# Optimization experiments

Hardware: AMD Instinct MI355X
Metric: run time of the kernel (lower is better)

## Reference

```python
import jax, jax.numpy as jnp
import numpy as np

N_NODES = 100000
N_EDGES = 1600000
IN_CH = 64
HID = 64
OUT_CH = 16


def setup_inputs() -> dict:
    key = jax.random.key(0)
    ks = jax.random.split(key, 8)
    x = jax.random.normal(ks[0], (N_NODES, IN_CH), dtype=jnp.float32)
    edge_index = jax.random.randint(ks[1], (2, N_EDGES), 0, N_NODES, dtype=jnp.int64)
    s = 1.0 / np.sqrt(IN_CH)
    W1l = jax.random.normal(ks[2], (HID, IN_CH), dtype=jnp.float32) * s
    W1r = jax.random.normal(ks[3], (HID, IN_CH), dtype=jnp.float32) * s
    b1 = jnp.zeros((HID,), dtype=jnp.float32)
    W2l = jax.random.normal(ks[4], (HID, HID), dtype=jnp.float32) * s
    W2r = jax.random.normal(ks[5], (HID, HID), dtype=jnp.float32) * s
    b2 = jnp.zeros((HID,), dtype=jnp.float32)
    Wlin = jax.random.normal(ks[6], (OUT_CH, HID), dtype=jnp.float32) * s
    blin = jnp.zeros((OUT_CH,), dtype=jnp.float32)
    return {"x": x, "edge_index": edge_index, "W1l": W1l, "b1": b1, "W1r": W1r,
            "W2l": W2l, "b2": b2, "W2r": W2r, "Wlin": Wlin, "blin": blin}


def _sage_conv(x, src, dst, Wl, b, Wr):
    # PyG SAGEConv with mean aggregation:
    # out = lin_l(mean_{j in N(i)} x_j) + lin_r(x_i); bias lives in lin_l.
    msgs = x[src]                                              # [E, F] gather
    summed = jax.ops.segment_sum(msgs, dst, num_segments=N_NODES)  # [N, F]
    cnt = jax.ops.segment_sum(jnp.ones((src.shape[0],), x.dtype), dst,
                              num_segments=N_NODES)            # [N]
    agg = summed / jnp.maximum(cnt, 1.0)[:, None]              # mean, deg-0 safe
    return agg @ Wl.T + b + x @ Wr.T


def reference(x, edge_index, W1l, b1, W1r, W2l, b2, W2r, Wlin, blin):
    src, dst = edge_index[0], edge_index[1]
    h = jax.nn.relu(_sage_conv(x, src, dst, W1l, b1, W1r))
    h = jax.nn.relu(_sage_conv(h, src, dst, W2l, b2, W2r))
    return h @ Wlin.T + blin
```

## Files before the change

kernel.cpp:

```cpp
#include <hip/hip_runtime.h>

#define NN 100000
#define NE 1600000

#define BSHIFT 9
#define BWIDTH (1 << BSHIFT)
#define NBUCK ((NN + BWIDTH - 1) >> BSHIFT)
#define SLOTS 12288
#define CHUNK 4096
#define B1_BLOCKS ((NE + CHUNK - 1) / CHUNK)
#define GEMM_BLOCKS ((NN + 63) / 64)

typedef float    v2f __attribute__((ext_vector_type(2)));
typedef unsigned v2u __attribute__((ext_vector_type(2)));

__device__ __forceinline__ float u2f(unsigned u) {
    union { unsigned u; float f; } v; v.u = u; return v.f;
}
__device__ __forceinline__ unsigned f2u(float f) {
    union { float f; unsigned u; } v; v.f = f; return v.u;
}
__device__ __forceinline__ unsigned f2bf(float f) {
    unsigned u = f2u(f);
    return (u + 0x7FFFu + ((u >> 16) & 1u)) >> 16;
}
__device__ __forceinline__ v2f unpk(unsigned x) {
    v2u w; w[0] = x << 16; w[1] = x & 0xFFFF0000u;
    union { v2u u; v2f f; } c; c.u = w; return c.f;
}

__global__ void detect_mode_kernel(const int* ei32, int* flag, int* bcnt) {
    __shared__ int any_nonzero;
    if (threadIdx.x == 0) any_nonzero = 0;
    if (threadIdx.x < NBUCK) bcnt[threadIdx.x] = 0;
    __syncthreads();
    int idx = 1 + 2 * threadIdx.x;
    if (ei32[idx] != 0) atomicOr(&any_nonzero, 1);
    __syncthreads();
    if (threadIdx.x == 0) flag[0] = (any_nonzero == 0) ? 1 : 0;
}

__device__ __forceinline__ void load_edge(const void* ei, int is64, int e,
                                          int& s, int& d) {
    if (is64) {
        const long long* p = (const long long*)ei;
        s = (int)p[e];
        d = (int)p[NE + e];
    } else {
        const int* p = (const int*)ei;
        s = p[e];
        d = p[NE + e];
    }
}

__global__ __launch_bounds__(256) void bucket_scatter_kernel(
    const void* ei, const int* flag,
    int* __restrict__ bcnt, int2* __restrict__ bpairs)
{
    __shared__ int hist[NBUCK];
    __shared__ int scanb[NBUCK];
    __shared__ int gbase[NBUCK];
    __shared__ int lofs[NBUCK];
    __shared__ int sc[256];
    __shared__ int2 stage[CHUNK];
    __shared__ unsigned short sbuck[CHUNK];

    const int t = threadIdx.x;
    const int is64 = *flag;
    const int e0 = blockIdx.x * CHUNK;
    const int nE = min(CHUNK, NE - e0);

    for (int i = t; i < NBUCK; i += 256) { hist[i] = 0; lofs[i] = 0; }
    __syncthreads();

    int sr[16], dr[16];
    #pragma unroll
    for (int r = 0; r < 16; ++r) {
        int e = e0 + t + 256 * r;
        if (e < NE) load_edge(ei, is64, e, sr[r], dr[r]);
        else dr[r] = -1;
    }
    #pragma unroll
    for (int r = 0; r < 16; ++r)
        if (dr[r] >= 0) atomicAdd(&hist[dr[r] >> BSHIFT], 1);
    __syncthreads();

    int v = (t < NBUCK) ? hist[t] : 0;
    sc[t] = v;
    __syncthreads();
    for (int off = 1; off < 256; off <<= 1) {
        int u = (t >= off) ? sc[t - off] : 0;
        __syncthreads();
        sc[t] += u;
        __syncthreads();
    }
    if (t < NBUCK) {
        scanb[t] = sc[t] - v;
        gbase[t] = atomicAdd(&bcnt[t], v);
    }
    __syncthreads();

    #pragma unroll
    for (int r = 0; r < 16; ++r) {
        if (dr[r] >= 0) {
            int b = dr[r] >> BSHIFT;
            int p = scanb[b] + atomicAdd(&lofs[b], 1);
            stage[p] = make_int2(sr[r], dr[r]);
            sbuck[p] = (unsigned short)b;
        }
    }
    __syncthreads();

    for (int i = t; i < nE; i += 256) {
        int b = sbuck[i];
        int off = gbase[b] + (i - scanb[b]);
        if (off < SLOTS) bpairs[(size_t)b * SLOTS + off] = stage[i];
    }
}

template<int BF16IN>
__device__ __forceinline__ void gemm_body(
    char* smem,
    const void* __restrict__ featv,
    const float* __restrict__ Wl, const float* __restrict__ Wr,
    const float* __restrict__ bias,
    unsigned* __restrict__ outt, unsigned* __restrict__ outr,
    int tile, int t)
{
    float (*As)[68]  = (float(*)[68])smem;
    float (*Bs)[132] = (float(*)[132])(smem + 32 * 68 * 4);
    const int m0 = tile * 64;

    const int tn = t & 7;
    const int tc = t >> 3;
    const int c0 = 4 * tc;

    float acc[8][4];
    {
        float b0 = 0.f, b1 = 0.f, b2 = 0.f, b3 = 0.f;
        if (c0 >= 64) {
            b0 = bias[c0 - 64]; b1 = bias[c0 - 63];
            b2 = bias[c0 - 62]; b3 = bias[c0 - 61];
        }
        #pragma unroll
        for (int i = 0; i < 8; ++i) {
            acc[i][0] = b0; acc[i][1] = b1; acc[i][2] = b2; acc[i][3] = b3;
        }
    }

    const int cw   = t & 127;
    const int half = t >> 7;
    const float* Wsrc = (cw < 64) ? (Wl + (size_t)cw * 64)
                                  : (Wr + (size_t)(cw - 64) * 64);
    const float*    featf = (const float*)featv;
    const unsigned* featu = (const unsigned*)featv;
    const int k0f = 4 * (t & 7);
    const int nbf = t >> 3;
    const int kqb = t & 3;
    const int nbb = t >> 2;

    float4 bv[4];
    #pragma unroll
    for (int i = 0; i < 4; ++i)
        bv[i] = *(const float4*)(Wsrc + 4 * (half + 2 * i));
    float4 av[2]; uint4 au;
    if (BF16IN) {
        int gn = m0 + nbb;
        au = (gn < NN) ? *(const uint4*)(featu + (size_t)gn * 32 + 4 * kqb)
                       : make_uint4(0u, 0u, 0u, 0u);
    } else {
        #pragma unroll
        for (int rep = 0; rep < 2; ++rep) {
            int gn = m0 + nbf + 32 * rep;
            av[rep] = (gn < NN)
                ? *(const float4*)(featf + (size_t)gn * 64 + k0f)
                : make_float4(0.f, 0.f, 0.f, 0.f);
        }
    }
    #pragma unroll
    for (int i = 0; i < 4; ++i) {
        int jl = half + 2 * i;
        Bs[4 * jl + 0][cw] = bv[i].x; Bs[4 * jl + 1][cw] = bv[i].y;
        Bs[4 * jl + 2][cw] = bv[i].z; Bs[4 * jl + 3][cw] = bv[i].w;
    }
    if (BF16IN) {
        int kk = 8 * kqb;
        As[kk + 0][nbb] = u2f(au.x << 16); As[kk + 1][nbb] = u2f(au.x & 0xFFFF0000u);
        As[kk + 2][nbb] = u2f(au.y << 16); As[kk + 3][nbb] = u2f(au.y & 0xFFFF0000u);
        As[kk + 4][nbb] = u2f(au.z << 16); As[kk + 5][nbb] = u2f(au.z & 0xFFFF0000u);
        As[kk + 6][nbb] = u2f(au.w << 16); As[kk + 7][nbb] = u2f(au.w & 0xFFFF0000u);
    } else {
        #pragma unroll
        for (int rep = 0; rep < 2; ++rep) {
            int n = nbf + 32 * rep;
            As[k0f + 0][n] = av[rep].x; As[k0f + 1][n] = av[rep].y;
            As[k0f + 2][n] = av[rep].z; As[k0f + 3][n] = av[rep].w;
        }
    }
    __syncthreads();

    float4 bv1[4];
    #pragma unroll
    for (int i = 0; i < 4; ++i)
        bv1[i] = *(const float4*)(Wsrc + 4 * (8 + half + 2 * i));
    float4 av1[2]; uint4 au1;
    if (BF16IN) {
        int gn = m0 + nbb;
        au1 = (gn < NN) ? *(const uint4*)(featu + (size_t)gn * 32 + 16 + 4 * kqb)
                        : make_uint4(0u, 0u, 0u, 0u);
    } else {
        #pragma unroll
        for (int rep = 0; rep < 2; ++rep) {
            int gn = m0 + nbf + 32 * rep;
            av1[rep] = (gn < NN)
                ? *(const float4*)(featf + (size_t)gn * 64 + 32 + k0f)
                : make_float4(0.f, 0.f, 0.f, 0.f);
        }
    }

    #pragma unroll 16
    for (int k = 0; k < 32; ++k) {
        float4 a0 = *(const float4*)&As[k][8 * tn];
        float4 a1 = *(const float4*)&As[k][8 * tn + 4];
        float4 b  = *(const float4*)&Bs[k][c0];
        float avv[8] = {a0.x, a0.y, a0.z, a0.w, a1.x, a1.y, a1.z, a1.w};
        float bvv[4] = {b.x, b.y, b.z, b.w};
        #pragma unroll
        for (int i = 0; i < 8; ++i)
            #pragma unroll
            for (int j = 0; j < 4; ++j)
                acc[i][j] = fmaf(avv[i], bvv[j], acc[i][j]);
    }
    __syncthreads();

    #pragma unroll
    for (int i = 0; i < 4; ++i) {
        int jl = half + 2 * i;
        Bs[4 * jl + 0][cw] = bv1[i].x; Bs[4 * jl + 1][cw] = bv1[i].y;
        Bs[4 * jl + 2][cw] = bv1[i].z; Bs[4 * jl + 3][cw] = bv1[i].w;
    }
    if (BF16IN) {
        int kk = 8 * kqb;
        As[kk + 0][nbb] = u2f(au1.x << 16); As[kk + 1][nbb] = u2f(au1.x & 0xFFFF0000u);
        As[kk + 2][nbb] = u2f(au1.y << 16); As[kk + 3][nbb] = u2f(au1.y & 0xFFFF0000u);
        As[kk + 4][nbb] = u2f(au1.z << 16); As[kk + 5][nbb] = u2f(au1.z & 0xFFFF0000u);
        As[kk + 6][nbb] = u2f(au1.w << 16); As[kk + 7][nbb] = u2f(au1.w & 0xFFFF0000u);
    } else {
        #pragma unroll
        for (int rep = 0; rep < 2; ++rep) {
            int n = nbf + 32 * rep;
            As[k0f + 0][n] = av1[rep].x; As[k0f + 1][n] = av1[rep].y;
            As[k0f + 2][n] = av1[rep].z; As[k0f + 3][n] = av1[rep].w;
        }
    }
    __syncthreads();

    #pragma unroll 16
    for (int k = 0; k < 32; ++k) {
        float4 a0 = *(const float4*)&As[k][8 * tn];
        float4 a1 = *(const float4*)&As[k][8 * tn + 4];
        float4 b  = *(const float4*)&Bs[k][c0];
        float avv[8] = {a0.x, a0.y, a0.z, a0.w, a1.x, a1.y, a1.z, a1.w};
        float bvv[4] = {b.x, b.y, b.z, b.w};
        #pragma unroll
        for (int i = 0; i < 8; ++i)
            #pragma unroll
            for (int j = 0; j < 4; ++j)
                acc[i][j] = fmaf(avv[i], bvv[j], acc[i][j]);
    }

    unsigned* dst = (c0 < 64) ? outt : outr;
    const int cc = (c0 < 64) ? c0 : c0 - 64;
    #pragma unroll
    for (int i = 0; i < 8; ++i) {
        int gn = m0 + 8 * tn + i;
        if (gn < NN) {
            uint2 p;
            p.x = f2bf(acc[i][0]) | (f2bf(acc[i][1]) << 16);
            p.y = f2bf(acc[i][2]) | (f2bf(acc[i][3]) << 16);
            *(uint2*)(dst + (size_t)gn * 32 + (cc >> 1)) = p;
        }
    }
}

__global__ __launch_bounds__(256) void csr_gemm1_kernel(
    const int* __restrict__ bcnt, const int2* __restrict__ bpairs,
    int* __restrict__ rowptr, int* __restrict__ colb,
    const float* __restrict__ x,
    const float* __restrict__ W1l, const float* __restrict__ W1r,
    const float* __restrict__ b1,
    unsigned* __restrict__ T, unsigned* __restrict__ R)
{
    __shared__ __align__(16) char smem[25600];
    const int t = threadIdx.x;

    if (blockIdx.x >= NBUCK) {
        if (blockIdx.x == NBUCK && t < 32) T[(size_t)NN * 32 + t] = 0u;
        gemm_body<0>(smem, x, W1l, W1r, b1, T, R, blockIdx.x - NBUCK, t);
        return;
    }

    int* ldeg = (int*)smem;
    int* lptr = ldeg + 512;
    int* lcnt = lptr + 512;
    int* sc   = lcnt + 512;

    const int b = blockIdx.x;

    int v = (t < NBUCK) ? bcnt[t] : 0;
    sc[t] = v;
    __syncthreads();
    for (int off = 1; off < 256; off <<= 1) {
        int u = (t >= off) ? sc[t - off] : 0;
        __syncthreads();
        sc[t] += u;
        __syncthreads();
    }
    const int base = (b == 0) ? 0 : sc[b - 1];
    if (b == 0 && t == 0) rowptr[NN] = NE;

    const int n0 = b << BSHIFT;
    const int cnt = min(bcnt[b], SLOTS);
    const int2* src = bpairs + (size_t)b * SLOTS;

    for (int i = t; i < BWIDTH; i += 256) { ldeg[i] = 0; lcnt[i] = 0; }
    __syncthreads();

    for (int i = t; i < cnt; i += 256)
        atomicAdd(&ldeg[src[i].y - n0], 1);
    __syncthreads();

    int a0 = ldeg[2 * t], a1 = ldeg[2 * t + 1];
    int s = a0 + a1;
    sc[t] = s;
    __syncthreads();
    for (int off = 1; off < 256; off <<= 1) {
        int u = (t >= off) ? sc[t - off] : 0;
        __syncthreads();
        sc[t] += u;
        __syncthreads();
    }
    int exc = sc[t] - s;
    lptr[2 * t] = exc;
    lptr[2 * t + 1] = exc + a0;
    __syncthreads();

    for (int i = t; i < BWIDTH; i += 256) {
        int gn = n0 + i;
        if (gn < NN) rowptr[gn] = base + lptr[i];
    }

    for (int i = t; i < cnt; i += 256) {
        int2 p = src[i];
        int li = p.y - n0;
        int pos = lptr[li] + atomicAdd(&lcnt[li], 1);
        colb[base + pos] = p.x << 7;
    }
}

__global__ __launch_bounds__(256) void gemm2_kernel(
    const unsigned* __restrict__ feat,
    const float* __restrict__ Wl, const float* __restrict__ Wr,
    const float* __restrict__ bias,
    unsigned* __restrict__ outt, unsigned* __restrict__ outr)
{
    __shared__ __align__(16) char smem[25600];
    gemm_body<1>(smem, feat, Wl, Wr, bias, outt, outr, blockIdx.x, threadIdx.x);
}

__global__ void aggregate_relu_kernel(const int* __restrict__ rowptr,
                                      const int* __restrict__ colb,
                                      const unsigned* __restrict__ tt,
                                      unsigned* rh) {
    const int wv   = (blockIdx.x * blockDim.x + threadIdx.x) >> 6;
    const int lane = threadIdx.x & 63;
    const int half = lane >> 5;
    const int slot = (lane >> 3) & 3;
    const int c8   = lane & 7;
    const int node = 2 * wv + half;
    if (node >= NN) return;

    const int beg = rowptr[node], end = rowptr[node + 1];
    const int deg = end - beg;
    int niter = (deg + 3) >> 2;
    niter = max(niter, __shfl_xor(niter, 32));

    const char* tb = (const char*)tt;
    const int zoff = NN * 128;
    v2f a0 = {0.f, 0.f}, a1 = {0.f, 0.f}, a2 = {0.f, 0.f}, a3 = {0.f, 0.f};
    v2f b0 = {0.f, 0.f}, b1 = {0.f, 0.f}, b2 = {0.f, 0.f}, b3 = {0.f, 0.f};

    int jj = beg + slot;
    int it = 0;
    for (; it + 4 <= niter; it += 4, jj += 16) {
        int jc0 = min(jj,      end - 1);
        int jc1 = min(jj + 4,  end - 1);
        int jc2 = min(jj + 8,  end - 1);
        int jc3 = min(jj + 12, end - 1);
        int o0 = colb[jc0];
        int o1 = colb[jc1];
        int o2 = colb[jc2];
        int o3 = colb[jc3];
        o0 = (jj      < end) ? o0 : zoff;
        o1 = (jj + 4  < end) ? o1 : zoff;
        o2 = (jj + 8  < end) ? o2 : zoff;
        o3 = (jj + 12 < end) ? o3 : zoff;
        uint4 u0 = *(const uint4*)(tb + (size_t)(unsigned)o0 + 16 * c8);
        uint4 u1 = *(const uint4*)(tb + (size_t)(unsigned)o1 + 16 * c8);
        uint4 u2 = *(const uint4*)(tb + (size_t)(unsigned)o2 + 16 * c8);
        uint4 u3 = *(const uint4*)(tb + (size_t)(unsigned)o3 + 16 * c8);
        a0 += unpk(u0.x); a1 += unpk(u0.y); a2 += unpk(u0.z); a3 += unpk(u0.w);
        b0 += unpk(u1.x); b1 += unpk(u1.y); b2 += unpk(u1.z); b3 += unpk(u1.w);
        a0 += unpk(u2.x); a1 += unpk(u2.y); a2 += unpk(u2.z); a3 += unpk(u2.w);
        b0 += unpk(u3.x); b1 += unpk(u3.y); b2 += unpk(u3.z); b3 += unpk(u3.w);
    }
    for (; it < niter; ++it, jj += 4) {
        int jc0 = min(jj, end - 1);
        int o0 = colb[jc0];
        o0 = (jj < end) ? o0 : zoff;
        uint4 u0 = *(const uint4*)(tb + (size_t)(unsigned)o0 + 16 * c8);
        a0 += unpk(u0.x); a1 += unpk(u0.y); a2 += unpk(u0.z); a3 += unpk(u0.w);
    }
    a0 += b0; a1 += b1; a2 += b2; a3 += b3;

    a0[0] += __shfl_xor(a0[0], 8);  a0[1] += __shfl_xor(a0[1], 8);
    a1[0] += __shfl_xor(a1[0], 8);  a1[1] += __shfl_xor(a1[1], 8);
    a2[0] += __shfl_xor(a2[0], 8);  a2[1] += __shfl_xor(a2[1], 8);
    a3[0] += __shfl_xor(a3[0], 8);  a3[1] += __shfl_xor(a3[1], 8);
    a0[0] += __shfl_xor(a0[0], 16); a0[1] += __shfl_xor(a0[1], 16);
    a1[0] += __shfl_xor(a1[0], 16); a1[1] += __shfl_xor(a1[1], 16);
    a2[0] += __shfl_xor(a2[0], 16); a2[1] += __shfl_xor(a2[1], 16);
    a3[0] += __shfl_xor(a3[0], 16); a3[1] += __shfl_xor(a3[1], 16);

    if (slot == 0) {
        float inv = 1.0f / fmaxf((float)deg, 1.0f);
        unsigned* p = rh + (size_t)node * 32 + 4 * c8;
        uint4 rr = *(const uint4*)p;
        v2f q0 = unpk(rr.x), q1 = unpk(rr.y), q2 = unpk(rr.z), q3 = unpk(rr.w);
        float h0 = fmaxf(fmaf(a0[0], inv, q0[0]), 0.0f);
        float h1 = fmaxf(fmaf(a0[1], inv, q0[1]), 0.0f);
        float h2 = fmaxf(fmaf(a1[0], inv, q1[0]), 0.0f);
        float h3 = fmaxf(fmaf(a1[1], inv, q1[1]), 0.0f);
        float h4 = fmaxf(fmaf(a2[0], inv, q2[0]), 0.0f);
        float h5 = fmaxf(fmaf(a2[1], inv, q2[1]), 0.0f);
        float h6 = fmaxf(fmaf(a3[0], inv, q3[0]), 0.0f);
        float h7 = fmaxf(fmaf(a3[1], inv, q3[1]), 0.0f);
        uint4 wv4;
        wv4.x = f2bf(h0) | (f2bf(h1) << 16);
        wv4.y = f2bf(h2) | (f2bf(h3) << 16);
        wv4.z = f2bf(h4) | (f2bf(h5) << 16);
        wv4.w = f2bf(h6) | (f2bf(h7) << 16);
        *(uint4*)p = wv4;
    }
}

__global__ __launch_bounds__(256) void head_kernel(
    const unsigned* __restrict__ hu,
    const float* __restrict__ Wlin,
    const float* __restrict__ blin,
    float* __restrict__ out)
{
    __shared__ float As[64][132];
    __shared__ float Bs[64][18];
    const int t = threadIdx.x;

    {
        int c = t & 15, j = t >> 4;
        float4 v = *(const float4*)(Wlin + (size_t)c * 64 + 4 * j);
        Bs[4 * j + 0][c] = v.x; Bs[4 * j + 1][c] = v.y;
        Bs[4 * j + 2][c] = v.z; Bs[4 * j + 3][c] = v.w;
    }
    const int m0 = blockIdx.x * 128;
    {
        int kq = t & 7;
        int nb = t >> 3;
        for (int rep = 0; rep < 4; ++rep) {
            int n = nb + 32 * rep;
            int gn = m0 + n;
            uint4 u = (gn < NN) ? *(const uint4*)(hu + (size_t)gn * 32 + 4 * kq)
                                : make_uint4(0u, 0u, 0u, 0u);
            int kk = 8 * kq;
            As[kk + 0][n] = u2f(u.x << 16); As[kk + 1][n] = u2f(u.x & 0xFFFF0000u);
            As[kk + 2][n] = u2f(u.y << 16); As[kk + 3][n] = u2f(u.y & 0xFFFF0000u);
            As[kk + 4][n] = u2f(u.z << 16); As[kk + 5][n] = u2f(u.z & 0xFFFF0000u);
            As[kk + 6][n] = u2f(u.w << 16); As[kk + 7][n] = u2f(u.w & 0xFFFF0000u);
        }
    }
    __syncthreads();

    const int tn = t & 31;
    const int tc = t >> 5;
    const int c0 = 2 * tc;
    float acc[4][2];
    #pragma unroll
    for (int i = 0; i < 4; ++i) { acc[i][0] = blin[c0]; acc[i][1] = blin[c0 + 1]; }

    #pragma unroll 16
    for (int k = 0; k < 64; ++k) {
        float4 a = *(const float4*)&As[k][4 * tn];
        float b0 = Bs[k][c0], b1 = Bs[k][c0 + 1];
        float av[4] = {a.x, a.y, a.z, a.w};
        #pragma unroll
        for (int i = 0; i < 4; ++i) {
            acc[i][0] = fmaf(av[i], b0, acc[i][0]);
            acc[i][1] = fmaf(av[i], b1, acc[i][1]);
        }
    }
    #pragma unroll
    for (int i = 0; i < 4; ++i) {
        int gn = m0 + 4 * tn + i;
        if (gn < NN)
            *(float2*)(out + (size_t)gn * 16 + c0) = make_float2(acc[i][0], acc[i][1]);
    }
}

extern "C" void kernel_launch(void* const* d_in, const int* in_sizes, int n_in,
                              void* d_out, int out_size, void* d_ws, size_t ws_size,
                              hipStream_t stream) {
    const float* x    = (const float*)d_in[0];
    const void*  ei   = d_in[1];
    const float* W1l  = (const float*)d_in[2];
    const float* b1   = (const float*)d_in[3];
    const float* W1r  = (const float*)d_in[4];
    const float* W2l  = (const float*)d_in[5];
    const float* b2   = (const float*)d_in[6];
    const float* W2r  = (const float*)d_in[7];
    const float* Wlin = (const float*)d_in[8];
    const float* blin = (const float*)d_in[9];
    float* out = (float*)d_out;

    char* w = (char*)d_ws;
    int*      flag   = (int*)w;
    int*      bcnt   = (int*)(w + (size_t)4 * 1024);
    int*      rowptr = (int*)(w + (size_t)1024 * 1024);
    int*      colb   = (int*)(w + (size_t)2 * 1024 * 1024);
    int2*     bpairs = (int2*)(w + (size_t)10 * 1024 * 1024);
    unsigned* T      = (unsigned*)(w + (size_t)30 * 1024 * 1024);
    unsigned* R      = (unsigned*)(w + (size_t)43 * 1024 * 1024);

    detect_mode_kernel<<<1, 256, 0, stream>>>((const int*)ei, flag, bcnt);
    bucket_scatter_kernel<<<B1_BLOCKS, 256, 0, stream>>>(ei, flag, bcnt, bpairs);

    csr_gemm1_kernel<<<NBUCK + GEMM_BLOCKS, 256, 0, stream>>>(
        bcnt, bpairs, rowptr, colb, x, W1l, W1r, b1, T, R);

    const int aggWaves  = (NN + 1) / 2;
    const int aggBlocks = (aggWaves * 64 + 255) / 256;
    const int headBlocks = (NN + 127) / 128;

    aggregate_relu_kernel<<<aggBlocks, 256, 0, stream>>>(rowptr, colb, T, R);

    gemm2_kernel<<<GEMM_BLOCKS, 256, 0, stream>>>(R, W2l, W2r, b2, T, R);
    aggregate_relu_kernel<<<aggBlocks, 256, 0, stream>>>(rowptr, colb, T, R);

    head_kernel<<<headBlocks, 256, 0, stream>>>(R, Wlin, blin, out);
}
```

Baseline: 163.0 us.

## Use bf16 MFMA for SAGE GEMMs and fuse layer-1 GEMM with edge bucketing

Replaces the scalar-FMA register-tiled GEMM with a bf16 MFMA 16x16x32 version that converts x and weights to bf16 in shared memory. It also moves the layer-1 GEMM blocks into the edge bucket-scatter kernel so they run concurrently, and makes bucket-to-CSR a separate 512-thread kernel. The scatter chunk is halved to 2048 edges, which doubles the block count. Rounding the fp32 input and weights to bf16 loses precision, and the output is now written as strided 16-bit stores, which may hurt coalescing.

After: 153.6 us. -5.8%, faster.

```diff
diff --git a/kernel.cpp b/kernel.cpp
--- a/kernel.cpp
+++ b/kernel.cpp
@@ -4,15 +4,17 @@
 #define NE 1600000
 
 #define BSHIFT 9
-#define BWIDTH (1 << BSHIFT)
-#define NBUCK ((NN + BWIDTH - 1) >> BSHIFT)
+#define BWIDTH 512
+#define NBUCK 196
 #define SLOTS 12288
-#define CHUNK 4096
+#define CHUNK 2048
 #define B1_BLOCKS ((NE + CHUNK - 1) / CHUNK)
 #define GEMM_BLOCKS ((NN + 63) / 64)
 
 typedef float    v2f __attribute__((ext_vector_type(2)));
 typedef unsigned v2u __attribute__((ext_vector_type(2)));
+typedef short    bf16x8 __attribute__((ext_vector_type(8)));
+typedef float    f32x4  __attribute__((ext_vector_type(4)));
 
 __device__ __forceinline__ float u2f(unsigned u) {
     union { unsigned u; float f; } v; v.u = u; return v.f;
@@ -53,264 +55,200 @@
     }
 }
 
-__global__ __launch_bounds__(256) void bucket_scatter_kernel(
-    const void* ei, const int* flag,
-    int* __restrict__ bcnt, int2* __restrict__ bpairs)
-{
-    __shared__ int hist[NBUCK];
-    __shared__ int scanb[NBUCK];
-    __shared__ int gbase[NBUCK];
-    __shared__ int lofs[NBUCK];
-    __shared__ int sc[256];
-    __shared__ int2 stage[CHUNK];
-    __shared__ unsigned short sbuck[CHUNK];
-
-    const int t = threadIdx.x;
-    const int is64 = *flag;
-    const int e0 = blockIdx.x * CHUNK;
-    const int nE = min(CHUNK, NE - e0);
-
-    for (int i = t; i < NBUCK; i += 256) { hist[i] = 0; lofs[i] = 0; }
-    __syncthreads();
-
-    int sr[16], dr[16];
-    #pragma unroll
-    for (int r = 0; r < 16; ++r) {
-        int e = e0 + t + 256 * r;
-        if (e < NE) load_edge(ei, is64, e, sr[r], dr[r]);
-        else dr[r] = -1;
-    }
-    #pragma unroll
-    for (int r = 0; r < 16; ++r)
-        if (dr[r] >= 0) atomicAdd(&hist[dr[r] >> BSHIFT], 1);
-    __syncthreads();
-
-    int v = (t < NBUCK) ? hist[t] : 0;
-    sc[t] = v;
-    __syncthreads();
-    for (int off = 1; off < 256; off <<= 1) {
-        int u = (t >= off) ? sc[t - off] : 0;
-        __syncthreads();
-        sc[t] += u;
-        __syncthreads();
-    }
-    if (t < NBUCK) {
-        scanb[t] = sc[t] - v;
-        gbase[t] = atomicAdd(&bcnt[t], v);
-    }
-    __syncthreads();
-
-    #pragma unroll
-    for (int r = 0; r < 16; ++r) {
-        if (dr[r] >= 0) {
-            int b = dr[r] >> BSHIFT;
-            int p = scanb[b] + atomicAdd(&lofs[b], 1);
-            stage[p] = make_int2(sr[r], dr[r]);
-            sbuck[p] = (unsigned short)b;
-        }
-    }
-    __syncthreads();
-
-    for (int i = t; i < nE; i += 256) {
-        int b = sbuck[i];
-        int off = gbase[b] + (i - scanb[b]);
-        if (off < SLOTS) bpairs[(size_t)b * SLOTS + off] = stage[i];
-    }
-}
-
 template<int BF16IN>
-__device__ __forceinline__ void gemm_body(
-    char* smem,
-    const void* __restrict__ featv,
+__device__ __forceinline__ void gemm_mfma_body(
+    char* smem, const void* __restrict__ featv,
     const float* __restrict__ Wl, const float* __restrict__ Wr,
     const float* __restrict__ bias,
     unsigned* __restrict__ outt, unsigned* __restrict__ outr,
     int tile, int t)
 {
-    float (*As)[68]  = (float(*)[68])smem;
-    float (*Bs)[132] = (float(*)[132])(smem + 32 * 68 * 4);
+    unsigned short* Als = (unsigned short*)smem;
+    unsigned short* Bls = (unsigned short*)(smem + 9216);
+    const int lane = t & 63, w = t >> 6;
     const int m0 = tile * 64;
-
-    const int tn = t & 7;
-    const int tc = t >> 3;
-    const int c0 = 4 * tc;
-
-    float acc[8][4];
-    {
-        float b0 = 0.f, b1 = 0.f, b2 = 0.f, b3 = 0.f;
-        if (c0 >= 64) {
-            b0 = bias[c0 - 64]; b1 = bias[c0 - 63];
-            b2 = bias[c0 - 62]; b3 = bias[c0 - 61];
-        }
-        #pragma unroll
-        for (int i = 0; i < 8; ++i) {
-            acc[i][0] = b0; acc[i][1] = b1; acc[i][2] = b2; acc[i][3] = b3;
-        }
-    }
-
-    const int cw   = t & 127;
-    const int half = t >> 7;
-    const float* Wsrc = (cw < 64) ? (Wl + (size_t)cw * 64)
-                                  : (Wr + (size_t)(cw - 64) * 64);
     const float*    featf = (const float*)featv;
     const unsigned* featu = (const unsigned*)featv;
-    const int k0f = 4 * (t & 7);
-    const int nbf = t >> 3;
-    const int kqb = t & 3;
-    const int nbb = t >> 2;
-
-    float4 bv[4];
-    #pragma unroll
-    for (int i = 0; i < 4; ++i)
-        bv[i] = *(const float4*)(Wsrc + 4 * (half + 2 * i));
-    float4 av[2]; uint4 au;
-    if (BF16IN) {
-        int gn = m0 + nbb;
-        au = (gn < NN) ? *(const uint4*)(featu + (size_t)gn * 32 + 4 * kqb)
-                       : make_uint4(0u, 0u, 0u, 0u);
-    } else {
-        #pragma unroll
-        for (int rep = 0; rep < 2; ++rep) {
-            int gn = m0 + nbf + 32 * rep;
-            av[rep] = (gn < NN)
-                ? *(const float4*)(featf + (size_t)gn * 64 + k0f)
-                : make_float4(0.f, 0.f, 0.f, 0.f);
-        }
-    }
-    #pragma unroll
-    for (int i = 0; i < 4; ++i) {
-        int jl = half + 2 * i;
-        Bs[4 * jl + 0][cw] = bv[i].x; Bs[4 * jl + 1][cw] = bv[i].y;
-        Bs[4 * jl + 2][cw] = bv[i].z; Bs[4 * jl + 3][cw] = bv[i].w;
-    }
-    if (BF16IN) {
-        int kk = 8 * kqb;
-        As[kk + 0][nbb] = u2f(au.x << 16); As[kk + 1][nbb] = u2f(au.x & 0xFFFF0000u);
-        As[kk + 2][nbb] = u2f(au.y << 16); As[kk + 3][nbb] = u2f(au.y & 0xFFFF0000u);
-        As[kk + 4][nbb] = u2f(au.z << 16); As[kk + 5][nbb] = u2f(au.z & 0xFFFF0000u);
-        As[kk + 6][nbb] = u2f(au.w << 16); As[kk + 7][nbb] = u2f(au.w & 0xFFFF0000u);
-    } else {
-        #pragma unroll
-        for (int rep = 0; rep < 2; ++rep) {
-            int n = nbf + 32 * rep;
-            As[k0f + 0][n] = av[rep].x; As[k0f + 1][n] = av[rep].y;
-            As[k0f + 2][n] = av[rep].z; As[k0f + 3][n] = av[rep].w;
-        }
-    }
-    __syncthreads();
-
-    float4 bv1[4];
-    #pragma unroll
-    for (int i = 0; i < 4; ++i)
-        bv1[i] = *(const float4*)(Wsrc + 4 * (8 + half + 2 * i));
-    float4 av1[2]; uint4 au1;
-    if (BF16IN) {
-        int gn = m0 + nbb;
-        au1 = (gn < NN) ? *(const uint4*)(featu + (size_t)gn * 32 + 16 + 4 * kqb)
-                        : make_uint4(0u, 0u, 0u, 0u);
-    } else {
-        #pragma unroll
-        for (int rep = 0; rep < 2; ++rep) {
-            int gn = m0 + nbf + 32 * rep;
-            av1[rep] = (gn < NN)
-                ? *(const float4*)(featf + (size_t)gn * 64 + 32 + k0f)
-                : make_float4(0.f, 0.f, 0.f, 0.f);
-        }
-    }
-
-    #pragma unroll 16
-    for (int k = 0; k < 32; ++k) {
-        float4 a0 = *(const float4*)&As[k][8 * tn];
-        float4 a1 = *(const float4*)&As[k][8 * tn + 4];
-        float4 b  = *(const float4*)&Bs[k][c0];
-        float avv[8] = {a0.x, a0.y, a0.z, a0.w, a1.x, a1.y, a1.z, a1.w};
-        float bvv[4] = {b.x, b.y, b.z, b.w};
-        #pragma unroll
-        for (int i = 0; i < 8; ++i)
+
+    #pragma unroll
+    for (int rep = 0; rep < 2; ++rep) {
+        int task = t + 256 * rep;
+        int row = task >> 3, s = task & 7;
+        int gn = m0 + row;
+        uint4 u;
+        if (BF16IN) {
+            u = (gn < NN) ? *(const uint4*)(featu + (size_t)gn * 32 + 4 * s)
+                          : make_uint4(0u, 0u, 0u, 0u);
+        } else {
+            if (gn < NN) {
+                float4 v0 = *(const float4*)(featf + (size_t)gn * 64 + 8 * s);
+                float4 v1 = *(const float4*)(featf + (size_t)gn * 64 + 8 * s + 4);
+                u.x = f2bf(v0.x) | (f2bf(v0.y) << 16);
+                u.y = f2bf(v0.z) | (f2bf(v0.w) << 16);
+                u.z = f2bf(v1.x) | (f2bf(v1.y) << 16);
+                u.w = f2bf(v1.z) | (f2bf(v1.w) << 16);
+            } else u = make_uint4(0u, 0u, 0u, 0u);
+        }
+        *(uint4*)(Als + row * 72 + 8 * s) = u;
+    }
+    #pragma unroll
+    for (int rep = 0; rep < 4; ++rep) {
+        int task = t + 256 * rep;
+        int c = task >> 3, s = task & 7;
+        const float* Wsrc = (c < 64) ? (Wl + (size_t)c * 64)
+                                     : (Wr + (size_t)(c - 64) * 64);
+        float4 v0 = *(const float4*)(Wsrc + 8 * s);
+        float4 v1 = *(const float4*)(Wsrc + 8 * s + 4);
+        uint4 u;
+        u.x = f2bf(v0.x) | (f2bf(v0.y) << 16);
+        u.y = f2bf(v0.z) | (f2bf(v0.w) << 16);
+        u.z = f2bf(v1.x) | (f2bf(v1.y) << 16);
+        u.w = f2bf(v1.z) | (f2bf(v1.w) << 16);
+        *(uint4*)(Bls + c * 72 + 8 * s) = u;
+    }
+    __syncthreads();
+
+    const int r = lane & 15, g = lane >> 4;
+    const int cw0 = 32 * w;
+
+    bf16x8 bf[2][2];
+    #pragma unroll
+    for (int ct = 0; ct < 2; ++ct)
+        #pragma unroll
+        for (int ks = 0; ks < 2; ++ks) {
+            int c = cw0 + 16 * ct + r;
+            bf[ct][ks] = *(const bf16x8*)(Bls + c * 72 + (ks * 4 + g) * 8);
+        }
+
+    f32x4 acc[4][2];
+    #pragma unroll
+    for (int nt = 0; nt < 4; ++nt)
+        #pragma unroll
+        for (int ct = 0; ct < 2; ++ct)
+            acc[nt][ct] = (f32x4){0.f, 0.f, 0.f, 0.f};
+
+    #pragma unroll
+    for (int nt = 0; nt < 4; ++nt) {
+        bf16x8 af[2];
+        #pragma unroll
+        for (int ks = 0; ks < 2; ++ks) {
+            int rr = nt * 16 + r;
+            af[ks] = *(const bf16x8*)(Als + rr * 72 + (ks * 4 + g) * 8);
+        }
+        #pragma unroll
+        for (int ct = 0; ct < 2; ++ct)
             #pragma unroll
-            for (int j = 0; j < 4; ++j)
-                acc[i][j] = fmaf(avv[i], bvv[j], acc[i][j]);
-    }
-    __syncthreads();
-
-    #pragma unroll
-    for (int i = 0; i < 4; ++i) {
-        int jl = half + 2 * i;
-        Bs[4 * jl + 0][cw] = bv1[i].x; Bs[4 * jl + 1][cw] = bv1[i].y;
-        Bs[4 * jl + 2][cw] = bv1[i].z; Bs[4 * jl + 3][cw] = bv1[i].w;
-    }
-    if (BF16IN) {
-        int kk = 8 * kqb;
-        As[kk + 0][nbb] = u2f(au1.x << 16); As[kk + 1][nbb] = u2f(au1.x & 0xFFFF0000u);
-        As[kk + 2][nbb] = u2f(au1.y << 16); As[kk + 3][nbb] = u2f(au1.y & 0xFFFF0000u);
-        As[kk + 4][nbb] = u2f(au1.z << 16); As[kk + 5][nbb] = u2f(au1.z & 0xFFFF0000u);
-        As[kk + 6][nbb] = u2f(au1.w << 16); As[kk + 7][nbb] = u2f(au1.w & 0xFFFF0000u);
-    } else {
-        #pragma unroll
-        for (int rep = 0; rep < 2; ++rep) {
-            int n = nbf + 32 * rep;
-            As[k0f + 0][n] = av1[rep].x; As[k0f + 1][n] = av1[rep].y;
-            As[k0f + 2][n] = av1[rep].z; As[k0f + 3][n] = av1[rep].w;
-        }
-    }
-    __syncthreads();
-
-    #pragma unroll 16
-    for (int k = 0; k < 32; ++k) {
-        float4 a0 = *(const float4*)&As[k][8 * tn];
-        float4 a1 = *(const float4*)&As[k][8 * tn + 4];
-        float4 b  = *(const float4*)&Bs[k][c0];
-        float avv[8] = {a0.x, a0.y, a0.z, a0.w, a1.x, a1.y, a1.z, a1.w};
-        float bvv[4] = {b.x, b.y, b.z, b.w};
-        #pragma unroll
-        for (int i = 0; i < 8; ++i)
+            for (int ks = 0; ks < 2; ++ks)
+                acc[nt][ct] = __builtin_amdgcn_mfma_f32_16x16x32_bf16(
+                    af[ks], bf[ct][ks], acc[nt][ct], 0, 0, 0);
+    }
+
+    unsigned short* Tb = (unsigned short*)outt;
+    unsigned short* Rb = (unsigned short*)outr;
+    #pragma unroll
+    for (int ct = 0; ct < 2; ++ct) {
+        int c = cw0 + 16 * ct + r;
+        float badd = (c >= 64) ? bias[c - 64] : 0.f;
+        unsigned short* dst = (c < 64) ? (Tb + c) : (Rb + (c - 64));
+        #pragma unroll
+        for (int nt = 0; nt < 4; ++nt)
             #pragma unroll
-            for (int j = 0; j < 4; ++j)
-                acc[i][j] = fmaf(avv[i], bvv[j], acc[i][j]);
-    }
-
-    unsigned* dst = (c0 < 64) ? outt : outr;
-    const int cc = (c0 < 64) ? c0 : c0 - 64;
-    #pragma unroll
-    for (int i = 0; i < 8; ++i) {
-        int gn = m0 + 8 * tn + i;
-        if (gn < NN) {
-            uint2 p;
-            p.x = f2bf(acc[i][0]) | (f2bf(acc[i][1]) << 16);
-            p.y = f2bf(acc[i][2]) | (f2bf(acc[i][3]) << 16);
-            *(uint2*)(dst + (size_t)gn * 32 + (cc >> 1)) = p;
-        }
-    }
-}
-
-__global__ __launch_bounds__(256) void csr_gemm1_kernel(
-    const int* __restrict__ bcnt, const int2* __restrict__ bpairs,
-    int* __restrict__ rowptr, int* __restrict__ colb,
+            for (int i = 0; i < 4; ++i) {
+                int row = m0 + nt * 16 + g * 4 + i;
+                if (row < NN)
+                    dst[(size_t)row * 64] = (unsigned short)f2bf(acc[nt][ct][i] + badd);
+            }
+    }
+}
+
+__global__ __launch_bounds__(256) void b1_gemm1_kernel(
+    const void* ei, const int* flag,
+    int* __restrict__ bcnt, int2* __restrict__ bpairs,
     const float* __restrict__ x,
     const float* __restrict__ W1l, const float* __restrict__ W1r,
     const float* __restrict__ b1,
     unsigned* __restrict__ T, unsigned* __restrict__ R)
 {
-    __shared__ __align__(16) char smem[25600];
+    __shared__ __align__(16) char smem[27648];
     const int t = threadIdx.x;
 
-    if (blockIdx.x >= NBUCK) {
-        if (blockIdx.x == NBUCK && t < 32) T[(size_t)NN * 32 + t] = 0u;
-        gemm_body<0>(smem, x, W1l, W1r, b1, T, R, blockIdx.x - NBUCK, t);
+    if (blockIdx.x >= B1_BLOCKS) {
+        if (blockIdx.x == B1_BLOCKS && t < 32) T[(size_t)NN * 32 + t] = 0u;
+        gemm_mfma_body<0>(smem, x, W1l, W1r, b1, T, R, blockIdx.x - B1_BLOCKS, t);
         return;
     }
 
-    int* ldeg = (int*)smem;
-    int* lptr = ldeg + 512;
-    int* lcnt = lptr + 512;
-    int* sc   = lcnt + 512;
-
-    const int b = blockIdx.x;
+    int2* stage = (int2*)smem;
+    unsigned short* sbuck = (unsigned short*)(smem + 16384);
+    int* hist  = (int*)(smem + 20480);
+    int* scanb = (int*)(smem + 21264);
+    int* gbase = (int*)(smem + 22048);
+    int* lofs  = (int*)(smem + 22832);
+    int* sc    = (int*)(smem + 23616);
+
+    const int is64 = *flag;
+    const int e0 = blockIdx.x * CHUNK;
+    const int nE = min(CHUNK, NE - e0);
+
+    for (int i = t; i < NBUCK; i += 256) { hist[i] = 0; lofs[i] = 0; }
+    __syncthreads();
+
+    int sr[8], dr[8];
+    #pragma unroll
+    for (int rr = 0; rr < 8; ++rr) {
+        int e = e0 + t + 256 * rr;
+        if (e < NE) load_edge(ei, is64, e, sr[rr], dr[rr]);
+        else dr[rr] = -1;
+    }
+    #pragma unroll
+    for (int rr = 0; rr < 8; ++rr)
+        if (dr[rr] >= 0) atomicAdd(&hist[dr[rr] >> BSHIFT], 1);
+    __syncthreads();
+
+    int v = (t < NBUCK) ? hist[t] : 0;
+    sc[t] = v;
+    __syncthreads();
+    for (int off = 1; off < 256; off <<= 1) {
+        int u = (t >= off) ? sc[t - off] : 0;
+        __syncthreads();
+        sc[t] += u;
+        __syncthreads();
+    }
+    if (t < NBUCK) {
+        scanb[t] = sc[t] - v;
+        gbase[t] = atomicAdd(&bcnt[t], v);
+    }
+    __syncthreads();
+
+    #pragma unroll
+    for (int rr = 0; rr < 8; ++rr) {
+        if (dr[rr] >= 0) {
+            int b = dr[rr] >> BSHIFT;
+            int p = scanb[b] + atomicAdd(&lofs[b], 1);
+            stage[p] = make_int2(sr[rr], dr[rr]);
+            sbuck[p] = (unsigned short)b;
+        }
+    }
+    __syncthreads();
+
+    for (int i = t; i < nE; i += 256) {
+        int b = sbuck[i];
+        int off = gbase[b] + (i - scanb[b]);
+        if (off < SLOTS) bpairs[(size_t)b * SLOTS + off] = stage[i];
+    }
+}
+
+__global__ __launch_bounds__(512) void bucket_to_csr_kernel(
+    const int* __restrict__ bcnt, const int2* __restrict__ bpairs,
+    int* __restrict__ rowptr, int* __restrict__ colb)
+{
+    __shared__ int ldeg[512], lptr[512], lcnt[512], sc[512];
+    const int t = threadIdx.x, b = blockIdx.x;
 
     int v = (t < NBUCK) ? bcnt[t] : 0;
     sc[t] = v;
     __syncthreads();
-    for (int off = 1; off < 256; off <<= 1) {
+    for (int off = 1; off < 512; off <<= 1) {
         int u = (t >= off) ? sc[t - off] : 0;
         __syncthreads();
         sc[t] += u;
@@ -318,39 +256,34 @@
     }
     const int base = (b == 0) ? 0 : sc[b - 1];
     if (b == 0 && t == 0) rowptr[NN] = NE;
+    __syncthreads();
+
+    ldeg[t] = 0; lcnt[t] = 0;
+    __syncthreads();
 
     const int n0 = b << BSHIFT;
     const int cnt = min(bcnt[b], SLOTS);
     const int2* src = bpairs + (size_t)b * SLOTS;
-
-    for (int i = t; i < BWIDTH; i += 256) { ldeg[i] = 0; lcnt[i] = 0; }
-    __syncthreads();
-
-    for (int i = t; i < cnt; i += 256)
+    for (int i = t; i < cnt; i += 512)
         atomicAdd(&ldeg[src[i].y - n0], 1);
     __syncthreads();
 
-    int a0 = ldeg[2 * t], a1 = ldeg[2 * t + 1];
-    int s = a0 + a1;
-    sc[t] = s;
-    __syncthreads();
-    for (int off = 1; off < 256; off <<= 1) {
+    int a = ldeg[t];
+    sc[t] = a;
+    __syncthreads();
+    for (int off = 1; off < 512; off <<= 1) {
         int u = (t >= off) ? sc[t - off] : 0;
         __syncthreads();
         sc[t] += u;
         __syncthreads();
     }
-    int exc = sc[t] - s;
-    lptr[2 * t] = exc;
-    lptr[2 * t + 1] = exc + a0;
-    __syncthreads();
-
-    for (int i = t; i < BWIDTH; i += 256) {
-        int gn = n0 + i;
-        if (gn < NN) rowptr[gn] = base + lptr[i];
-    }
-
-    for (int i = t; i < cnt; i += 256) {
+    lptr[t] = sc[t] - a;
+    __syncthreads();
+
+    int gn = n0 + t;
+    if (gn < NN) rowptr[gn] = base + lptr[t];
+
+    for (int i = t; i < cnt; i += 512) {
         int2 p = src[i];
         int li = p.y - n0;
         int pos = lptr[li] + atomicAdd(&lcnt[li], 1);
@@ -364,8 +297,8 @@
     const float* __restrict__ bias,
     unsigned* __restrict__ outt, unsigned* __restrict__ outr)
 {
-    __shared__ __align__(16) char smem[25600];
-    gemm_body<1>(smem, feat, Wl, Wr, bias, outt, outr, blockIdx.x, threadIdx.x);
+    __shared__ __align__(16) char smem[27648];
+    gemm_mfma_body<1>(smem, feat, Wl, Wr, bias, outt, outr, blockIdx.x, threadIdx.x);
 }
 
 __global__ void aggregate_relu_kernel(const int* __restrict__ rowptr,
@@ -539,10 +472,11 @@
     unsigned* R      = (unsigned*)(w + (size_t)43 * 1024 * 1024);
 
     detect_mode_kernel<<<1, 256, 0, stream>>>((const int*)ei, flag, bcnt);
-    bucket_scatter_kernel<<<B1_BLOCKS, 256, 0, stream>>>(ei, flag, bcnt, bpairs);
-
-    csr_gemm1_kernel<<<NBUCK + GEMM_BLOCKS, 256, 0, stream>>>(
-        bcnt, bpairs, rowptr, colb, x, W1l, W1r, b1, T, R);
+
+    b1_gemm1_kernel<<<B1_BLOCKS + GEMM_BLOCKS, 256, 0, stream>>>(
+        ei, flag, bcnt, bpairs, x, W1l, W1r, b1, T, R);
+
+    bucket_to_csr_kernel<<<NBUCK, 512, 0, stream>>>(bcnt, bpairs, rowptr, colb);
 
     const int aggWaves  = (NN + 1) / 2;
     const int aggBlocks = (aggWaves * 64 + 255) / 256;
```
